# Optimization experiments

Measured on AMD Instinct MI355X. Metric: run time of the kernel, lower is better.

Reference implementation:

```python
import jax, jax.numpy as jnp
import numpy as np

TOP_K = 2

def setup_inputs() -> dict:
    key = jax.random.key(0)
    ks = jax.random.split(key, 8)
    B, S, H, I, E = 1, 2048, 2048, 8192, 8
    s = 0.02
    return {
        "hidden_states": jax.random.normal(ks[0], (B, S, H), jnp.float32),
        "gate_w": jax.random.normal(ks[1], (H, E), jnp.float32) * s,
        "gate_b": jnp.zeros((E,), jnp.float32),
        "fc1_w": jax.random.normal(ks[2], (E, H, I), jnp.float32) * s,
        "fc1_b": jnp.zeros((E, I), jnp.float32),
        "fc2_w": jax.random.normal(ks[3], (E, I, H), jnp.float32) * s,
        "fc2_b": jnp.zeros((E, H), jnp.float32),
        "alpha": jax.random.normal(ks[4], (E,), jnp.float32),
    }

def reference(hidden_states, gate_w, gate_b, fc1_w, fc1_b, fc2_w, fc2_b, alpha):
    B, S, H = hidden_states.shape
    E = alpha.shape[0]
    x = hidden_states.reshape(-1, H)  # [T, H]

    # GShard-style gate: linear -> softmax -> top-k
    logits = x @ gate_w + gate_b              # [T, E]
    scores = jax.nn.softmax(logits, axis=-1)  # [T, E]
    top_v, top_i = jax.lax.top_k(scores, TOP_K)  # [T, K]

    # Dense per-token combine weight per expert: sum_k onehot(idx_k) * score_k, scaled by alpha[e]
    gates = jnp.sum(jax.nn.one_hot(top_i, E, dtype=x.dtype) * top_v[..., None], axis=1)  # [T, E]
    gates = gates * alpha[None, :]

    # Per-expert MLP applied to all tokens (math identical to masked dispatch+combine)
    h1 = jax.nn.gelu(jnp.einsum('th,ehi->eti', x, fc1_w) + fc1_b[:, None, :], approximate=True)  # [E, T, I]
    out_all = jnp.einsum('eti,eih->eth', h1, fc2_w) + fc2_b[:, None, :]                          # [E, T, H]
    out = jnp.einsum('eth,te->th', out_all, gates)  # weighted combine [T, H]
    return out.reshape(B, S, H)
```

## Files before the change

### kernel.cpp

```cpp
#include <hip/hip_runtime.h>
#include <hip/hip_bf16.h>
#include <cstdint>

#define T_TOK 2048
#define HDIM  2048
#define IDIM  8192
#define NEXP  8

typedef short s16x8 __attribute__((ext_vector_type(8)));
typedef float f32x4 __attribute__((ext_vector_type(4)));

__device__ __forceinline__ unsigned short f2b(float f) {
    union { float f; unsigned u; } c; c.f = f;
    unsigned r = (c.u + 0x7fffu + ((c.u >> 16) & 1u)) >> 16;
    return (unsigned short)r;
}

__device__ __forceinline__ float gelu_tanh(float v) {
    float u = 0.7978845608028654f * (v + 0.044715f * v * v * v);
    return 0.5f * v * (1.0f + tanhf(u));
}

__global__ __launch_bounds__(256) void k_gate(
    const float* __restrict__ x, const float* __restrict__ gw,
    const float* __restrict__ gb, const float* __restrict__ alpha,
    unsigned short* __restrict__ xb, int* __restrict__ counts,
    int* __restrict__ top_e, float* __restrict__ top_g)
{
    const int wave = threadIdx.x >> 6;
    const int lane = threadIdx.x & 63;
    const int t = blockIdx.x * 4 + wave;
    if (t >= T_TOK) return;

    float acc[8];
    #pragma unroll
    for (int e = 0; e < 8; e++) acc[e] = 0.f;

    const float* xrow = x + (size_t)t * HDIM;
    unsigned short* xbrow = xb + (size_t)t * HDIM;

    #pragma unroll
    for (int c = 0; c < 8; c++) {
        const int h0 = c * 256 + lane * 4;
        const float4 xv = *reinterpret_cast<const float4*>(xrow + h0);
        ushort4 u;
        u.x = f2b(xv.x); u.y = f2b(xv.y); u.z = f2b(xv.z); u.w = f2b(xv.w);
        *reinterpret_cast<ushort4*>(xbrow + h0) = u;
        const float xs[4] = {xv.x, xv.y, xv.z, xv.w};
        #pragma unroll
        for (int r = 0; r < 4; r++) {
            const float4 g0 = *reinterpret_cast<const float4*>(gw + (size_t)(h0 + r) * 8);
            const float4 g1 = *reinterpret_cast<const float4*>(gw + (size_t)(h0 + r) * 8 + 4);
            acc[0] += xs[r] * g0.x; acc[1] += xs[r] * g0.y;
            acc[2] += xs[r] * g0.z; acc[3] += xs[r] * g0.w;
            acc[4] += xs[r] * g1.x; acc[5] += xs[r] * g1.y;
            acc[6] += xs[r] * g1.z; acc[7] += xs[r] * g1.w;
        }
    }
    #pragma unroll
    for (int e = 0; e < 8; e++) {
        #pragma unroll
        for (int off = 32; off > 0; off >>= 1)
            acc[e] += __shfl_xor(acc[e], off);
        acc[e] += gb[e];
    }
    float m = acc[0];
    #pragma unroll
    for (int e = 1; e < 8; e++) m = fmaxf(m, acc[e]);
    float Z = 0.f;
    #pragma unroll
    for (int e = 0; e < 8; e++) Z += expf(acc[e] - m);
    int e0 = 0; float b0 = acc[0];
    #pragma unroll
    for (int e = 1; e < 8; e++) if (acc[e] > b0) { b0 = acc[e]; e0 = e; }
    int e1 = -1; float b1 = -1e30f;
    #pragma unroll
    for (int e = 0; e < 8; e++) if (e != e0 && acc[e] > b1) { b1 = acc[e]; e1 = e; }

    if (lane == 0) {
        const float s0 = expf(b0 - m) / Z * alpha[e0];
        const float s1 = expf(b1 - m) / Z * alpha[e1];
        top_e[2 * t]     = e0; top_e[2 * t + 1] = e1;
        top_g[2 * t]     = s0; top_g[2 * t + 1] = s1;
        atomicAdd(&counts[e0], 1);
        atomicAdd(&counts[e1], 1);
    }
}

__global__ void k_scan(const int* __restrict__ counts, int* __restrict__ offsets,
                       int* __restrict__ cursors)
{
    if (threadIdx.x == 0) {
        int off = 0;
        for (int e = 0; e < NEXP; e++) {
            offsets[e] = off; cursors[e] = off; off += counts[e];
        }
    }
}

__global__ __launch_bounds__(256) void k_append(
    const int* __restrict__ top_e, const float* __restrict__ top_g,
    int* __restrict__ cursors, int* __restrict__ slot_token,
    float* __restrict__ slot_gate, int* __restrict__ tok2slot)
{
    const int t = blockIdx.x * 256 + threadIdx.x;
    if (t >= T_TOK) return;
    #pragma unroll
    for (int k = 0; k < 2; k++) {
        const int e = top_e[2 * t + k];
        const int slot = atomicAdd(&cursors[e], 1);
        slot_token[slot] = t;
        slot_gate[slot]  = top_g[2 * t + k];
        tok2slot[2 * t + k] = slot;
    }
}

__global__ __launch_bounds__(256) void k_fc1(
    const unsigned short* __restrict__ xb, const float* __restrict__ w1,
    const float* __restrict__ b1, const int* __restrict__ counts,
    const int* __restrict__ offsets, const int* __restrict__ slot_token,
    unsigned short* __restrict__ h1)
{
    const int e   = blockIdx.z;
    const int cnt = counts[e];
    const int m0  = blockIdx.y * 128;
    if (m0 >= cnt) return;
    const int moff = offsets[e];
    const int n0   = blockIdx.x * 128;

    __shared__ short As[128 * 40];
    __shared__ short Bs[128 * 40];
    __shared__ int row_tok[128];

    const int tid = threadIdx.x;
    if (tid < 128)
        row_tok[tid] = (m0 + tid < cnt) ? slot_token[moff + m0 + tid] : 0;
    __syncthreads();

    const int wave = tid >> 6, lane = tid & 63;
    const int wm = wave >> 1, wn = wave & 1;
    const int lo = lane & 15, hi = lane >> 4;

    f32x4 acc[4][4];
    #pragma unroll
    for (int i = 0; i < 4; i++)
        #pragma unroll
        for (int j = 0; j < 4; j++) acc[i][j] = (f32x4)0.f;

    const float* wbase = w1 + (size_t)e * HDIM * IDIM + n0;

    for (int kk = 0; kk < HDIM; kk += 32) {
        #pragma unroll
        for (int it = 0; it < 2; it++) {
            const int id = tid + it * 256;
            const int row = id >> 2, kg = id & 3;
            const int tok = row_tok[row];
            const s16x8 av = *reinterpret_cast<const s16x8*>(
                xb + (size_t)tok * HDIM + kk + kg * 8);
            *reinterpret_cast<s16x8*>(&As[row * 40 + kg * 8]) = av;
        }
        #pragma unroll
        for (int it = 0; it < 2; it++) {
            const int id = tid + it * 256;
            const int n = id & 127, kg = id >> 7;
            s16x8 bv;
            #pragma unroll
            for (int j = 0; j < 8; j++) {
                const float f = wbase[(size_t)(kk + kg * 8 + j) * IDIM + n];
                bv[j] = (short)f2b(f);
            }
            *reinterpret_cast<s16x8*>(&Bs[n * 40 + kg * 8]) = bv;
        }
        __syncthreads();
        s16x8 af[4], bfr[4];
        #pragma unroll
        for (int i = 0; i < 4; i++)
            af[i] = *reinterpret_cast<const s16x8*>(&As[(wm * 64 + i * 16 + lo) * 40 + hi * 8]);
        #pragma unroll
        for (int j = 0; j < 4; j++)
            bfr[j] = *reinterpret_cast<const s16x8*>(&Bs[(wn * 64 + j * 16 + lo) * 40 + hi * 8]);
        #pragma unroll
        for (int i = 0; i < 4; i++)
            #pragma unroll
            for (int j = 0; j < 4; j++)
                acc[i][j] = __builtin_amdgcn_mfma_f32_16x16x32_bf16(af[i], bfr[j], acc[i][j], 0, 0, 0);
        __syncthreads();
    }

    #pragma unroll
    for (int i = 0; i < 4; i++) {
        #pragma unroll
        for (int r = 0; r < 4; r++) {
            const int row = wm * 64 + i * 16 + hi * 4 + r;
            if (m0 + row >= cnt) continue;
            const size_t orow = (size_t)(moff + m0 + row) * IDIM;
            #pragma unroll
            for (int j = 0; j < 4; j++) {
                const int col = n0 + wn * 64 + j * 16 + lo;
                const float v = acc[i][j][r] + b1[e * IDIM + col];
                h1[orow + col] = f2b(gelu_tanh(v));
            }
        }
    }
}

__global__ __launch_bounds__(256) void k_fc2(
    const unsigned short* __restrict__ h1, const float* __restrict__ w2,
    const float* __restrict__ b2, const int* __restrict__ counts,
    const int* __restrict__ offsets, const float* __restrict__ slot_gate,
    float* __restrict__ outslot)
{
    const int e   = blockIdx.z;
    const int cnt = counts[e];
    const int m0  = blockIdx.y * 128;
    if (m0 >= cnt) return;
    const int moff = offsets[e];
    const int n0   = blockIdx.x * 128;
    const int slot0 = moff + m0;

    __shared__ short As[128 * 40];
    __shared__ short Bs[128 * 40];
    __shared__ float grow[128];

    const int tid = threadIdx.x;
    if (tid < 128)
        grow[tid] = (m0 + tid < cnt) ? slot_gate[slot0 + tid] : 0.f;

    const int wave = tid >> 6, lane = tid & 63;
    const int wm = wave >> 1, wn = wave & 1;
    const int lo = lane & 15, hi = lane >> 4;

    f32x4 acc[4][4];
    #pragma unroll
    for (int i = 0; i < 4; i++)
        #pragma unroll
        for (int j = 0; j < 4; j++) acc[i][j] = (f32x4)0.f;

    const float* wbase = w2 + (size_t)e * IDIM * HDIM + n0;

    for (int kk = 0; kk < IDIM; kk += 32) {
        #pragma unroll
        for (int it = 0; it < 2; it++) {
            const int id = tid + it * 256;
            const int row = id >> 2, kg = id & 3;
            const s16x8 av = *reinterpret_cast<const s16x8*>(
                h1 + (size_t)(slot0 + row) * IDIM + kk + kg * 8);
            *reinterpret_cast<s16x8*>(&As[row * 40 + kg * 8]) = av;
        }
        #pragma unroll
        for (int it = 0; it < 2; it++) {
            const int id = tid + it * 256;
            const int n = id & 127, kg = id >> 7;
            s16x8 bv;
            #pragma unroll
            for (int j = 0; j < 8; j++) {
                const float f = wbase[(size_t)(kk + kg * 8 + j) * HDIM + n];
                bv[j] = (short)f2b(f);
            }
            *reinterpret_cast<s16x8*>(&Bs[n * 40 + kg * 8]) = bv;
        }
        __syncthreads();
        s16x8 af[4], bfr[4];
        #pragma unroll
        for (int i = 0; i < 4; i++)
            af[i] = *reinterpret_cast<const s16x8*>(&As[(wm * 64 + i * 16 + lo) * 40 + hi * 8]);
        #pragma unroll
        for (int j = 0; j < 4; j++)
            bfr[j] = *reinterpret_cast<const s16x8*>(&Bs[(wn * 64 + j * 16 + lo) * 40 + hi * 8]);
        #pragma unroll
        for (int i = 0; i < 4; i++)
            #pragma unroll
            for (int j = 0; j < 4; j++)
                acc[i][j] = __builtin_amdgcn_mfma_f32_16x16x32_bf16(af[i], bfr[j], acc[i][j], 0, 0, 0);
        __syncthreads();
    }

    #pragma unroll
    for (int i = 0; i < 4; i++) {
        #pragma unroll
        for (int r = 0; r < 4; r++) {
            const int row = wm * 64 + i * 16 + hi * 4 + r;
            if (m0 + row >= cnt) continue;
            const float g = grow[row];
            const size_t orow = (size_t)(slot0 + row) * HDIM;
            #pragma unroll
            for (int j = 0; j < 4; j++) {
                const int col = n0 + wn * 64 + j * 16 + lo;
                outslot[orow + col] = g * (acc[i][j][r] + b2[e * HDIM + col]);
            }
        }
    }
}

__global__ __launch_bounds__(256) void k_combine(
    const float* __restrict__ outslot, const int* __restrict__ tok2slot,
    float* __restrict__ out)
{
    const int t = blockIdx.x;
    const int sA = tok2slot[2 * t], sB = tok2slot[2 * t + 1];
    const float* ra = outslot + (size_t)sA * HDIM;
    const float* rb = outslot + (size_t)sB * HDIM;
    float* ro = out + (size_t)t * HDIM;
    #pragma unroll
    for (int c = 0; c < 2; c++) {
        const int i = c * 1024 + threadIdx.x * 4;
        const float4 a = *reinterpret_cast<const float4*>(ra + i);
        const float4 b = *reinterpret_cast<const float4*>(rb + i);
        float4 o; o.x = a.x + b.x; o.y = a.y + b.y; o.z = a.z + b.z; o.w = a.w + b.w;
        *reinterpret_cast<float4*>(ro + i) = o;
    }
}

extern "C" void kernel_launch(void* const* d_in, const int* in_sizes, int n_in,
                              void* d_out, int out_size, void* d_ws, size_t ws_size,
                              hipStream_t stream)
{
    const float* x  = (const float*)d_in[0];
    const float* gw = (const float*)d_in[1];
    const float* gb = (const float*)d_in[2];
    const float* w1 = (const float*)d_in[3];
    const float* b1 = (const float*)d_in[4];
    const float* w2 = (const float*)d_in[5];
    const float* b2 = (const float*)d_in[6];
    const float* al = (const float*)d_in[7];
    float* out = (float*)d_out;

    char* ws = (char*)d_ws;
    unsigned short* xb = (unsigned short*)ws;
    unsigned short* h1 = (unsigned short*)(ws + 8388608);
    float* outslot     = (float*)(ws + 75497472);
    char* meta = ws + 109051904;
    int* counts     = (int*)meta;
    int* offsets    = (int*)(meta + 32);
    int* cursors    = (int*)(meta + 64);
    int* slot_token = (int*)(meta + 256);
    int* tok2slot   = (int*)(meta + 256 + 16384);
    int* top_e      = (int*)(meta + 256 + 32768);
    float* slot_gate= (float*)(meta + 256 + 49152);
    float* top_g    = (float*)(meta + 256 + 65536);

    hipMemsetAsync(counts, 0, 32, stream);
    k_gate<<<dim3(T_TOK / 4), dim3(256), 0, stream>>>(x, gw, gb, al, xb, counts, top_e, top_g);
    k_scan<<<dim3(1), dim3(64), 0, stream>>>(counts, offsets, cursors);
    k_append<<<dim3(T_TOK / 256), dim3(256), 0, stream>>>(top_e, top_g, cursors,
                                                          slot_token, slot_gate, tok2slot);
    k_fc1<<<dim3(IDIM / 128, T_TOK / 128, NEXP), dim3(256), 0, stream>>>(
        xb, w1, b1, counts, offsets, slot_token, h1);
    k_fc2<<<dim3(HDIM / 128, T_TOK / 128, NEXP), dim3(256), 0, stream>>>(
        h1, w2, b2, counts, offsets, slot_gate, outslot);
    k_combine<<<dim3(T_TOK), dim3(256), 0, stream>>>(outslot, tok2slot, out);
}
```

Measured before the change: 857.7 us.

## Rewrite grouped expert GEMMs with direct-to-LDS loads, vectorized weight reads, swizzled LDS

Merges the two expert GEMM kernels into one templated kernel. The activation tile now goes straight from global memory into LDS through global_load_lds. Weight tiles are read as float4 along N and packed to bf16 pairs, replacing strided scalar loads. K-tiles double to 64, LDS layouts use XOR swizzling to avoid bank conflicts, and a 1D grid is remapped so neighbouring blocks go to different XCDs. The aim is to cut global-load inefficiency on the fp32 weights and LDS conflicts, at the cost of more LDS per block and more complex indexing.

```diff
diff --git a/kernel.cpp b/kernel.cpp
--- a/kernel.cpp
+++ b/kernel.cpp
@@ -9,11 +9,20 @@
 
 typedef short s16x8 __attribute__((ext_vector_type(8)));
 typedef float f32x4 __attribute__((ext_vector_type(4)));
+typedef uint32_t u32x2 __attribute__((ext_vector_type(2)));
+typedef const __attribute__((address_space(1))) uint32_t gbl_u32;
+typedef __attribute__((address_space(3))) uint32_t lds_u32;
 
 __device__ __forceinline__ unsigned short f2b(float f) {
     union { float f; unsigned u; } c; c.f = f;
     unsigned r = (c.u + 0x7fffu + ((c.u >> 16) & 1u)) >> 16;
     return (unsigned short)r;
+}
+
+__device__ __forceinline__ uint32_t pk_bf16(float a, float b) {
+    union { __hip_bfloat162 h; uint32_t u; } c;
+    c.h = __float22bfloat162_rn(make_float2(a, b));
+    return c.u;
 }
 
 __device__ __forceinline__ float gelu_tanh(float v) {
@@ -115,75 +124,126 @@
     }
 }
 
-__global__ __launch_bounds__(256) void k_fc1(
-    const unsigned short* __restrict__ xb, const float* __restrict__ w1,
-    const float* __restrict__ b1, const int* __restrict__ counts,
-    const int* __restrict__ offsets, const int* __restrict__ slot_token,
-    unsigned short* __restrict__ h1)
-{
-    const int e   = blockIdx.z;
+template<bool FC1>
+__global__ __launch_bounds__(256) void k_gemm(
+    const unsigned short* __restrict__ Abase,
+    const float* __restrict__ W,
+    const float* __restrict__ bias,
+    const int* __restrict__ counts,
+    const int* __restrict__ offsets,
+    const int* __restrict__ slot_token,
+    const float* __restrict__ slot_gate,
+    unsigned short* __restrict__ out_bf,
+    float* __restrict__ out_f)
+{
+    constexpr int N  = FC1 ? IDIM : HDIM;
+    constexpr int K  = FC1 ? HDIM : IDIM;
+    constexpr int NT = N / 128;
+    constexpr int MT = T_TOK / 128;
+
+    constexpr int nwg = NEXP * NT * MT;
+    constexpr int cpx = nwg >> 3;
+    const int bid = blockIdx.x;
+    const int wg  = (bid & 7) * cpx + (bid >> 3);
+    const int e   = wg / (NT * MT);
+    const int rem = wg - e * (NT * MT);
+    const int nb  = rem / MT;
+    const int mb  = rem - nb * MT;
+
     const int cnt = counts[e];
-    const int m0  = blockIdx.y * 128;
+    const int m0  = mb * 128;
     if (m0 >= cnt) return;
-    const int moff = offsets[e];
-    const int n0   = blockIdx.x * 128;
-
-    __shared__ short As[128 * 40];
-    __shared__ short Bs[128 * 40];
-    __shared__ int row_tok[128];
-
-    const int tid = threadIdx.x;
-    if (tid < 128)
-        row_tok[tid] = (m0 + tid < cnt) ? slot_token[moff + m0 + tid] : 0;
-    __syncthreads();
-
-    const int wave = tid >> 6, lane = tid & 63;
+    const int moff  = offsets[e];
+    const int n0    = nb * 128;
+    const int slot0 = moff + m0;
+
+    __shared__ short    As[128 * 64];
+    __shared__ uint32_t Bs[128 * 36 + 2];
+
+    const int tid  = threadIdx.x;
+    const int lane = tid & 63, wave = tid >> 6;
     const int wm = wave >> 1, wn = wave & 1;
     const int lo = lane & 15, hi = lane >> 4;
 
+    const unsigned short* asrc[4];
+    #pragma unroll
+    for (int it = 0; it < 4; it++) {
+        const int row = (tid >> 3) + it * 32;
+        int tok;
+        if (FC1) tok = (m0 + row < cnt) ? slot_token[moff + m0 + row] : 0;
+        else     tok = slot0 + ((m0 + row < cnt) ? row : 0);
+        asrc[it] = Abase + (size_t)tok * K;
+    }
+    const int achunk = tid & 7;
+
+    const float* wcol = W + (size_t)e * K * N + n0;
+
     f32x4 acc[4][4];
     #pragma unroll
     for (int i = 0; i < 4; i++)
         #pragma unroll
         for (int j = 0; j < 4; j++) acc[i][j] = (f32x4)0.f;
 
-    const float* wbase = w1 + (size_t)e * HDIM * IDIM + n0;
-
-    for (int kk = 0; kk < HDIM; kk += 32) {
-        #pragma unroll
-        for (int it = 0; it < 2; it++) {
-            const int id = tid + it * 256;
-            const int row = id >> 2, kg = id & 3;
-            const int tok = row_tok[row];
-            const s16x8 av = *reinterpret_cast<const s16x8*>(
-                xb + (size_t)tok * HDIM + kk + kg * 8);
-            *reinterpret_cast<s16x8*>(&As[row * 40 + kg * 8]) = av;
-        }
-        #pragma unroll
-        for (int it = 0; it < 2; it++) {
-            const int id = tid + it * 256;
-            const int n = id & 127, kg = id >> 7;
-            s16x8 bv;
+    for (int kk = 0; kk < K; kk += 64) {
+        #pragma unroll
+        for (int it = 0; it < 4; it++) {
+            const int row = (tid >> 3) + it * 32;
+            const int sc  = achunk ^ (row & 7);
+            __builtin_amdgcn_global_load_lds(
+                (gbl_u32*)(asrc[it] + kk + sc * 8),
+                (lds_u32*)(As + (tid + it * 256) * 8), 16, 0, 0);
+        }
+        #pragma unroll
+        for (int u = 0; u < 2; u++) {
+            const int id = tid + u * 256;
+            const int kq = id >> 5;
+            const int k  = kq * 4;
+            const int n4 = (id & 31) * 4;
+            float w0[4], w1[4], w2r[4], w3[4];
+            {
+                const float4 a = *reinterpret_cast<const float4*>(wcol + (size_t)(kk + k    ) * N + n4);
+                const float4 b = *reinterpret_cast<const float4*>(wcol + (size_t)(kk + k + 1) * N + n4);
+                const float4 c = *reinterpret_cast<const float4*>(wcol + (size_t)(kk + k + 2) * N + n4);
+                const float4 d = *reinterpret_cast<const float4*>(wcol + (size_t)(kk + k + 3) * N + n4);
+                w0[0]=a.x; w0[1]=a.y; w0[2]=a.z; w0[3]=a.w;
+                w1[0]=b.x; w1[1]=b.y; w1[2]=b.z; w1[3]=b.w;
+                w2r[0]=c.x; w2r[1]=c.y; w2r[2]=c.z; w2r[3]=c.w;
+                w3[0]=d.x; w3[1]=d.y; w3[2]=d.z; w3[3]=d.w;
+            }
             #pragma unroll
-            for (int j = 0; j < 8; j++) {
-                const float f = wbase[(size_t)(kk + kg * 8 + j) * IDIM + n];
-                bv[j] = (short)f2b(f);
-            }
-            *reinterpret_cast<s16x8*>(&Bs[n * 40 + kg * 8]) = bv;
+            for (int dn = 0; dn < 4; dn++) {
+                const int n = n4 + dn;
+                const int chunk = (kq >> 1) ^ ((n >> 2) & 7);
+                u32x2 pk;
+                pk.x = pk_bf16(w0[dn], w1[dn]);
+                pk.y = pk_bf16(w2r[dn], w3[dn]);
+                *reinterpret_cast<u32x2*>(Bs + n * 36 + chunk * 4 + (kq & 1) * 2) = pk;
+            }
         }
         __syncthreads();
-        s16x8 af[4], bfr[4];
-        #pragma unroll
-        for (int i = 0; i < 4; i++)
-            af[i] = *reinterpret_cast<const s16x8*>(&As[(wm * 64 + i * 16 + lo) * 40 + hi * 8]);
-        #pragma unroll
-        for (int j = 0; j < 4; j++)
-            bfr[j] = *reinterpret_cast<const s16x8*>(&Bs[(wn * 64 + j * 16 + lo) * 40 + hi * 8]);
-        #pragma unroll
-        for (int i = 0; i < 4; i++)
+        #pragma unroll
+        for (int ks = 0; ks < 2; ks++) {
+            s16x8 af[4];
             #pragma unroll
-            for (int j = 0; j < 4; j++)
-                acc[i][j] = __builtin_amdgcn_mfma_f32_16x16x32_bf16(af[i], bfr[j], acc[i][j], 0, 0, 0);
+            for (int i = 0; i < 4; i++) {
+                const int arow = wm * 64 + i * 16 + lo;
+                const int ch = (ks * 4 + hi) ^ (arow & 7);
+                af[i] = *reinterpret_cast<const s16x8*>(As + arow * 64 + ch * 8);
+            }
+            s16x8 bfr[4];
+            #pragma unroll
+            for (int j = 0; j < 4; j++) {
+                const int coln = wn * 64 + j * 16 + lo;
+                const int chp  = (ks * 4 + hi) ^ ((coln >> 2) & 7);
+                bfr[j] = *reinterpret_cast<const s16x8*>(Bs + coln * 36 + chp * 4);
+            }
+            #pragma unroll
+            for (int i = 0; i < 4; i++)
+                #pragma unroll
+                for (int j = 0; j < 4; j++)
+                    acc[i][j] = __builtin_amdgcn_mfma_f32_16x16x32_bf16(
+                        af[i], bfr[j], acc[i][j], 0, 0, 0);
+        }
         __syncthreads();
     }
 
@@ -193,100 +253,22 @@
         for (int r = 0; r < 4; r++) {
             const int row = wm * 64 + i * 16 + hi * 4 + r;
             if (m0 + row >= cnt) continue;
-            const size_t orow = (size_t)(moff + m0 + row) * IDIM;
-            #pragma unroll
-            for (int j = 0; j < 4; j++) {
-                const int col = n0 + wn * 64 + j * 16 + lo;
-                const float v = acc[i][j][r] + b1[e * IDIM + col];
-                h1[orow + col] = f2b(gelu_tanh(v));
-            }
-        }
-    }
-}
-
-__global__ __launch_bounds__(256) void k_fc2(
-    const unsigned short* __restrict__ h1, const float* __restrict__ w2,
-    const float* __restrict__ b2, const int* __restrict__ counts,
-    const int* __restrict__ offsets, const float* __restrict__ slot_gate,
-    float* __restrict__ outslot)
-{
-    const int e   = blockIdx.z;
-    const int cnt = counts[e];
-    const int m0  = blockIdx.y * 128;
-    if (m0 >= cnt) return;
-    const int moff = offsets[e];
-    const int n0   = blockIdx.x * 128;
-    const int slot0 = moff + m0;
-
-    __shared__ short As[128 * 40];
-    __shared__ short Bs[128 * 40];
-    __shared__ float grow[128];
-
-    const int tid = threadIdx.x;
-    if (tid < 128)
-        grow[tid] = (m0 + tid < cnt) ? slot_gate[slot0 + tid] : 0.f;
-
-    const int wave = tid >> 6, lane = tid & 63;
-    const int wm = wave >> 1, wn = wave & 1;
-    const int lo = lane & 15, hi = lane >> 4;
-
-    f32x4 acc[4][4];
-    #pragma unroll
-    for (int i = 0; i < 4; i++)
-        #pragma unroll
-        for (int j = 0; j < 4; j++) acc[i][j] = (f32x4)0.f;
-
-    const float* wbase = w2 + (size_t)e * IDIM * HDIM + n0;
-
-    for (int kk = 0; kk < IDIM; kk += 32) {
-        #pragma unroll
-        for (int it = 0; it < 2; it++) {
-            const int id = tid + it * 256;
-            const int row = id >> 2, kg = id & 3;
-            const s16x8 av = *reinterpret_cast<const s16x8*>(
-                h1 + (size_t)(slot0 + row) * IDIM + kk + kg * 8);
-            *reinterpret_cast<s16x8*>(&As[row * 40 + kg * 8]) = av;
-        }
-        #pragma unroll
-        for (int it = 0; it < 2; it++) {
-            const int id = tid + it * 256;
-            const int n = id & 127, kg = id >> 7;
-            s16x8 bv;
-            #pragma unroll
-            for (int j = 0; j < 8; j++) {
-                const float f = wbase[(size_t)(kk + kg * 8 + j) * HDIM + n];
-                bv[j] = (short)f2b(f);
-            }
-            *reinterpret_cast<s16x8*>(&Bs[n * 40 + kg * 8]) = bv;
-        }
-        __syncthreads();
-        s16x8 af[4], bfr[4];
-        #pragma unroll
-        for (int i = 0; i < 4; i++)
-            af[i] = *reinterpret_cast<const s16x8*>(&As[(wm * 64 + i * 16 + lo) * 40 + hi * 8]);
-        #pragma unroll
-        for (int j = 0; j < 4; j++)
-            bfr[j] = *reinterpret_cast<const s16x8*>(&Bs[(wn * 64 + j * 16 + lo) * 40 + hi * 8]);
-        #pragma unroll
-        for (int i = 0; i < 4; i++)
-            #pragma unroll
-            for (int j = 0; j < 4; j++)
-                acc[i][j] = __builtin_amdgcn_mfma_f32_16x16x32_bf16(af[i], bfr[j], acc[i][j], 0, 0, 0);
-        __syncthreads();
-    }
-
-    #pragma unroll
-    for (int i = 0; i < 4; i++) {
-        #pragma unroll
-        for (int r = 0; r < 4; r++) {
-            const int row = wm * 64 + i * 16 + hi * 4 + r;
-            if (m0 + row >= cnt) continue;
-            const float g = grow[row];
-            const size_t orow = (size_t)(slot0 + row) * HDIM;
-            #pragma unroll
-            for (int j = 0; j < 4; j++) {
-                const int col = n0 + wn * 64 + j * 16 + lo;
-                outslot[orow + col] = g * (acc[i][j][r] + b2[e * HDIM + col]);
+            if (FC1) {
+                const size_t orow = (size_t)(slot0 + row) * IDIM;
+                #pragma unroll
+                for (int j = 0; j < 4; j++) {
+                    const int col = n0 + wn * 64 + j * 16 + lo;
+                    const float v = acc[i][j][r] + bias[e * N + col];
+                    out_bf[orow + col] = f2b(gelu_tanh(v));
+                }
+            } else {
+                const float g = slot_gate[slot0 + row];
+                const size_t orow = (size_t)(slot0 + row) * HDIM;
+                #pragma unroll
+                for (int j = 0; j < 4; j++) {
+                    const int col = n0 + wn * 64 + j * 16 + lo;
+                    out_f[orow + col] = g * (acc[i][j][r] + bias[e * N + col]);
+                }
             }
         }
     }
@@ -344,9 +326,9 @@
     k_scan<<<dim3(1), dim3(64), 0, stream>>>(counts, offsets, cursors);
     k_append<<<dim3(T_TOK / 256), dim3(256), 0, stream>>>(top_e, top_g, cursors,
                                                           slot_token, slot_gate, tok2slot);
-    k_fc1<<<dim3(IDIM / 128, T_TOK / 128, NEXP), dim3(256), 0, stream>>>(
-        xb, w1, b1, counts, offsets, slot_token, h1);
-    k_fc2<<<dim3(HDIM / 128, T_TOK / 128, NEXP), dim3(256), 0, stream>>>(
-        h1, w2, b2, counts, offsets, slot_gate, outslot);
+    k_gemm<true><<<dim3(NEXP * (IDIM / 128) * (T_TOK / 128)), dim3(256), 0, stream>>>(
+        xb, w1, b1, counts, offsets, slot_token, slot_gate, h1, nullptr);
+    k_gemm<false><<<dim3(NEXP * (HDIM / 128) * (T_TOK / 128)), dim3(256), 0, stream>>>(
+        h1, w2, b2, counts, offsets, slot_token, slot_gate, nullptr, outslot);
     k_combine<<<dim3(T_TOK), dim3(256), 0, stream>>>(outslot, tok2slot, out);
 }
```

After: 1.133 ms. +32.1%, slower.
